# Optimization experiments

Measured on AMD Instinct MI355X. Metric: run time of the kernel, lower is better.

Reference implementation:

```python
import jax, jax.numpy as jnp
import numpy as np

B, S, D_IN, D_OUT = 4, 2048, 1024, 1024

def setup_inputs() -> dict:
    key = jax.random.key(0)
    k1, k2, k3, k4 = jax.random.split(key, 4)
    x = jax.random.normal(k1, (B, S, D_IN), dtype=jnp.float32)
    # torch Linear weight is [d_out, d_in]; store as [d_in, d_out] for x @ W
    scale = 1.0 / np.sqrt(D_IN)
    Wq = jax.random.normal(k2, (D_IN, D_OUT), dtype=jnp.float32) * scale
    Wk = jax.random.normal(k3, (D_IN, D_OUT), dtype=jnp.float32) * scale
    Wv = jax.random.normal(k4, (D_IN, D_OUT), dtype=jnp.float32) * scale
    return {"x": x, "Wq": Wq, "Wk": Wk, "Wv": Wv}

def reference(x, Wq, Wk, Wv):
    b, n, _ = x.shape
    q = jnp.einsum('bnd,de->bne', x, Wq)
    k = jnp.einsum('bnd,de->bne', x, Wk)
    v = jnp.einsum('bnd,de->bne', x, Wv)
    scores = jnp.einsum('bqe,bke->bqk', q, k) / jnp.sqrt(jnp.float32(k.shape[-1]))
    causal = jnp.tril(jnp.ones((n, n), dtype=bool))  # True = keep
    scores = jnp.where(causal[None], scores, -jnp.inf)
    attn = jax.nn.softmax(scores, axis=-1)
    # dropout p=0.0 -> identity (eval-equivalent)
    return jnp.einsum('bqk,bke->bqe', attn, v)
```

## Files before the change

kernel.cpp:

```cpp
#include <hip/hip_runtime.h>
#include <hip/hip_bf16.h>
#include <math.h>

typedef __hip_bfloat16 bf16;
typedef __attribute__((ext_vector_type(8))) short short8;
typedef __attribute__((ext_vector_type(4))) float f32x4;

#define GLD16(gp, lp)                                                          \
    __builtin_amdgcn_global_load_lds(                                          \
        (const __attribute__((address_space(1))) unsigned int*)(gp),           \
        (__attribute__((address_space(3))) unsigned int*)(lp), 16, 0, 0)


__global__ __launch_bounds__(256) void cvt_x(const float* __restrict__ in,
                                             bf16* __restrict__ out) {
    long base = ((long)blockIdx.x * 256 + threadIdx.x) * 8;
    const float4* p = (const float4*)(in + base);
    float4 a = p[0], b = p[1];
    union { bf16 h[8]; short8 v; } o;
    o.h[0] = __float2bfloat16(a.x); o.h[1] = __float2bfloat16(a.y);
    o.h[2] = __float2bfloat16(a.z); o.h[3] = __float2bfloat16(a.w);
    o.h[4] = __float2bfloat16(b.x); o.h[5] = __float2bfloat16(b.y);
    o.h[6] = __float2bfloat16(b.z); o.h[7] = __float2bfloat16(b.w);
    *(short8*)(out + base) = o.v;
}

__global__ __launch_bounds__(256) void cvt_w_t(const float* __restrict__ Wq,
                                               const float* __restrict__ Wk,
                                               const float* __restrict__ Wv,
                                               bf16* __restrict__ WT) {
    const float* W = blockIdx.z == 0 ? Wq : (blockIdx.z == 1 ? Wk : Wv);
    bf16* T = WT + (long)blockIdx.z * 1024 * 1024;
    __shared__ float t[32][33];
    int n0 = blockIdx.x * 32, k0 = blockIdx.y * 32;
    int tx = threadIdx.x, ty = threadIdx.y;
    #pragma unroll
    for (int i = 0; i < 4; ++i)
        t[ty * 4 + i][tx] = W[(long)(k0 + ty * 4 + i) * 1024 + n0 + tx];
    __syncthreads();
    #pragma unroll
    for (int i = 0; i < 4; ++i)
        T[(long)(n0 + ty * 4 + i) * 1024 + k0 + tx] =
            __float2bfloat16(t[tx][ty * 4 + i]);
}

template <int MODE>
__global__ __launch_bounds__(256) void gemm_bt(
    const bf16* __restrict__ A, const bf16* __restrict__ B,
    void* __restrict__ C0, void* __restrict__ C1, void* __restrict__ C2,
    float* __restrict__ RS, int lda, int ldb, float alpha, long az, long bz) {
    int tm, tn, bi = 0;
    if (MODE == 1) {
        tn = blockIdx.x; tm = blockIdx.y;
    } else if (MODE == 0) {
        int t = blockIdx.x % 136;
        bi = blockIdx.x / 136;
        int i = (int)((sqrtf(8.f * t + 1.f) - 1.f) * 0.5f);
        while ((i + 1) * (i + 2) / 2 <= t) ++i;
        while (i * (i + 1) / 2 > t) --i;
        tm = i; tn = t - i * (i + 1) / 2;
    } else {
        tm = 15 - (int)(blockIdx.x >> 5);
        int r = blockIdx.x & 31;
        tn = r & 7; bi = r >> 3;
    }
    const int nk = (MODE == 2) ? 2 * (tm + 1) : 16;
    A += (long)bi * az;
    B += (long)bi * bz;

    const int m0 = tm * 128, n0 = tn * 128;
    __shared__ bf16 As[128 * 64];
    __shared__ bf16 Bs[128 * 64];

    const int tid = threadIdx.x;
    const int wave = tid >> 6, lane = tid & 63;
    const int wr = wave >> 1, wc = wave & 1;
    const int lrow = lane & 15, kg = lane >> 4;

    f32x4 acc[4][4];
    #pragma unroll
    for (int i = 0; i < 4; ++i)
        #pragma unroll
        for (int j = 0; j < 4; ++j) acc[i][j] = (f32x4){0.f, 0.f, 0.f, 0.f};

    const int srow = tid >> 3;
    const int scol = (((tid & 7) ^ (srow & 7)) << 3);
    const bf16* ap = A + (long)(m0 + srow) * lda + scol;
    const bf16* bp = B + (long)(n0 + srow) * ldb + scol;
    char* asb = (char*)As + tid * 16;
    char* bsb = (char*)Bs + tid * 16;

    for (int t = 0; t < nk; ++t) {
        const int k0 = t << 6;
        GLD16(ap + k0, asb);
        GLD16(ap + 32L * lda + k0, asb + 4096);
        GLD16(ap + 64L * lda + k0, asb + 8192);
        GLD16(ap + 96L * lda + k0, asb + 12288);
        GLD16(bp + k0, bsb);
        GLD16(bp + 32L * ldb + k0, bsb + 4096);
        GLD16(bp + 64L * ldb + k0, bsb + 8192);
        GLD16(bp + 96L * ldb + k0, bsb + 12288);
        __syncthreads();
        #pragma unroll
        for (int kk = 0; kk < 2; ++kk) {
            short8 af[4], bfr[4];
            #pragma unroll
            for (int mi = 0; mi < 4; ++mi) {
                const int rr = wr * 64 + mi * 16 + lrow;
                const int ch = ((kk << 2) | kg) ^ (rr & 7);
                af[mi] = *(const short8*)(&As[rr * 64 + (ch << 3)]);
            }
            #pragma unroll
            for (int ni = 0; ni < 4; ++ni) {
                const int rr = wc * 64 + ni * 16 + lrow;
                const int ch = ((kk << 2) | kg) ^ (rr & 7);
                bfr[ni] = *(const short8*)(&Bs[rr * 64 + (ch << 3)]);
            }
            #pragma unroll
            for (int mi = 0; mi < 4; ++mi)
                #pragma unroll
                for (int ni = 0; ni < 4; ++ni)
                    acc[mi][ni] = __builtin_amdgcn_mfma_f32_16x16x32_bf16(
                        af[mi], bfr[ni], acc[mi][ni], 0, 0, 0);
        }
        __syncthreads();
    }

    const int rb = wr * 64 + (lane >> 4) * 4;
    const int cb = wc * 64 + (lane & 15);
    if (MODE == 0) {
        bf16* E = (bf16*)C0 + (long)bi * 4194304;
        float* rsb = RS + bi * 2048;
        #pragma unroll
        for (int mi = 0; mi < 4; ++mi)
            #pragma unroll
            for (int j = 0; j < 4; ++j) {
                const int gq = m0 + rb + mi * 16 + j;
                float rp = 0.f;
                #pragma unroll
                for (int ni = 0; ni < 4; ++ni) {
                    const int gk = n0 + cb + ni * 16;
                    float e = (gk <= gq) ? __expf(acc[mi][ni][j] * alpha) : 0.f;
                    E[(long)gq * 2048 + gk] = __float2bfloat16(e);
                    rp += e;
                }
                #pragma unroll
                for (int o = 1; o < 16; o <<= 1) rp += __shfl_xor(rp, o);
                if ((lane & 15) == 0) atomicAdd(rsb + gq, rp);
            }
    } else if (MODE == 2) {
        float* Cf = (float*)C0 + (long)bi * 2097152;
        const float* rsb = RS + bi * 2048;
        #pragma unroll
        for (int mi = 0; mi < 4; ++mi)
            #pragma unroll
            for (int j = 0; j < 4; ++j) {
                const int gq = m0 + rb + mi * 16 + j;
                const float inv = 1.f / rsb[gq];
                #pragma unroll
                for (int ni = 0; ni < 4; ++ni)
                    Cf[(long)gq * 1024 + (n0 + cb + ni * 16)] =
                        acc[mi][ni][j] * inv;
            }
    } else {
        const int sel = n0 >> 10;
        const int nb = n0 & 1023;
        if (sel < 2) {
            bf16* Cb = sel ? (bf16*)C1 : (bf16*)C0;
            #pragma unroll
            for (int mi = 0; mi < 4; ++mi)
                #pragma unroll
                for (int ni = 0; ni < 4; ++ni)
                    #pragma unroll
                    for (int j = 0; j < 4; ++j)
                        Cb[(long)(m0 + rb + mi * 16 + j) * 1024 + (nb + cb + ni * 16)] =
                            __float2bfloat16(acc[mi][ni][j]);
        } else {
            bf16* T = (bf16*)C2;
            #pragma unroll
            for (int mi = 0; mi < 4; ++mi)
                #pragma unroll
                for (int ni = 0; ni < 4; ++ni) {
                    int gm = m0 + rb + mi * 16;
                    int col = nb + cb + ni * 16;
                    int b = gm >> 11, mm = gm & 2047;
                    union { bf16 h[4]; ushort4 v; } o;
                    #pragma unroll
                    for (int j = 0; j < 4; ++j)
                        o.h[j] = __float2bfloat16(acc[mi][ni][j]);
                    *(ushort4*)(T + (long)b * 2097152 + (long)col * 2048 + mm) = o.v;
                }
        }
    }
}

extern "C" void kernel_launch(void* const* d_in, const int* in_sizes, int n_in,
                              void* d_out, int out_size, void* d_ws,
                              size_t ws_size, hipStream_t stream) {
    const float* x = (const float*)d_in[0];
    const float* Wq = (const float*)d_in[1];
    const float* Wk = (const float*)d_in[2];
    const float* Wv = (const float*)d_in[3];
    float* out = (float*)d_out;

    char* ws = (char*)d_ws;
    bf16* xb = (bf16*)ws;
    bf16* wt = (bf16*)(ws + 16777216);
    bf16* Qb = (bf16*)(ws + 23068672);
    bf16* Kb = (bf16*)(ws + 39845888);
    bf16* VT = (bf16*)(ws + 56623104);
    bf16* E  = (bf16*)(ws + 73400320);
    float* rs = (float*)(ws + 106954752);
    if (ws_size < 106987520) return;

    cvt_x<<<4096, 256, 0, stream>>>(x, xb);
    cvt_w_t<<<dim3(32, 32, 3), dim3(32, 8), 0, stream>>>(Wq, Wk, Wv, wt);
    hipMemsetAsync(rs, 0, 4 * 2048 * sizeof(float), stream);
    gemm_bt<1><<<dim3(24, 64), 256, 0, stream>>>(
        xb, wt, Qb, Kb, VT, nullptr, 1024, 1024, 1.f, 0, 0);
    gemm_bt<0><<<544, 256, 0, stream>>>(
        Qb, Kb, E, nullptr, nullptr, rs, 1024, 1024, 0.03125f, 2097152,
        2097152);
    gemm_bt<2><<<512, 256, 0, stream>>>(
        E, VT, out, nullptr, nullptr, rs, 2048, 2048, 1.f, 4194304, 2097152);
}
```

Before: 251.1 us.

## Use 512-thread 256x256 tiles with triple-buffered LDS pipeline in GEMMs

Measured after the change: 229.4 us. -8.6%, faster.

```diff
diff --git a/kernel.cpp b/kernel.cpp
--- a/kernel.cpp
+++ b/kernel.cpp
@@ -44,8 +44,8 @@
             __float2bfloat16(t[tx][ty * 4 + i]);
 }
 
-template <int MODE>
-__global__ __launch_bounds__(256) void gemm_bt(
+template <int MODE, int MF>
+__global__ __launch_bounds__(512, 2) void gemm8p(
     const bf16* __restrict__ A, const bf16* __restrict__ B,
     void* __restrict__ C0, void* __restrict__ C1, void* __restrict__ C2,
     float* __restrict__ RS, int lda, int ldb, float alpha, long az, long bz) {
@@ -53,86 +53,123 @@
     if (MODE == 1) {
         tn = blockIdx.x; tm = blockIdx.y;
     } else if (MODE == 0) {
-        int t = blockIdx.x % 136;
-        bi = blockIdx.x / 136;
+        int t = blockIdx.x % 36;
+        bi = blockIdx.x / 36;
         int i = (int)((sqrtf(8.f * t + 1.f) - 1.f) * 0.5f);
         while ((i + 1) * (i + 2) / 2 <= t) ++i;
         while (i * (i + 1) / 2 > t) --i;
         tm = i; tn = t - i * (i + 1) / 2;
     } else {
-        tm = 15 - (int)(blockIdx.x >> 5);
-        int r = blockIdx.x & 31;
-        tn = r & 7; bi = r >> 3;
+        tm = 15 - (int)(blockIdx.x >> 4);
+        int r = blockIdx.x & 15;
+        tn = r & 3; bi = r >> 2;
     }
-    const int nk = (MODE == 2) ? 2 * (tm + 1) : 16;
+    const int BM = MF * 32;
+    const int nk = (MODE == 2) ? 4 * (tm + 1) : 32;
     A += (long)bi * az;
     B += (long)bi * bz;
-
-    const int m0 = tm * 128, n0 = tn * 128;
-    __shared__ bf16 As[128 * 64];
-    __shared__ bf16 Bs[128 * 64];
+    const int m0 = tm * BM, n0 = tn * 256;
+
+    const int ABUF = MF * 1024;
+    __shared__ bf16 lds[3 * (MF * 1024 + 8192)];
+    bf16* Ab[3] = {lds, lds + ABUF, lds + 2 * ABUF};
+    bf16* Bb[3] = {lds + 3 * ABUF, lds + 3 * ABUF + 8192, lds + 3 * ABUF + 16384};
 
     const int tid = threadIdx.x;
     const int wave = tid >> 6, lane = tid & 63;
-    const int wr = wave >> 1, wc = wave & 1;
+    const int wr = wave >> 2, wc = wave & 3;
     const int lrow = lane & 15, kg = lane >> 4;
 
-    f32x4 acc[4][4];
+    f32x4 acc[MF][4];
     #pragma unroll
-    for (int i = 0; i < 4; ++i)
+    for (int i = 0; i < MF; ++i)
         #pragma unroll
         for (int j = 0; j < 4; ++j) acc[i][j] = (f32x4){0.f, 0.f, 0.f, 0.f};
 
-    const int srow = tid >> 3;
-    const int scol = (((tid & 7) ^ (srow & 7)) << 3);
+    const int srow = tid >> 2;
+    const int scol = ((((srow >> 1) & 3) ^ (tid & 3)) << 3);
     const bf16* ap = A + (long)(m0 + srow) * lda + scol;
     const bf16* bp = B + (long)(n0 + srow) * ldb + scol;
-    char* asb = (char*)As + tid * 16;
-    char* bsb = (char*)Bs + tid * 16;
+
+    #define STAGE_A(buf, kof)                                                  \
+        { char* d = (char*)(buf) + tid * 16;                                   \
+          GLD16(ap + (kof), d);                                                \
+          if (MF == 8) GLD16(ap + 128L * lda + (kof), d + 8192); }
+    #define STAGE_B(buf, kof)                                                  \
+        { char* d = (char*)(buf) + tid * 16;                                   \
+          GLD16(bp + (kof), d);                                                \
+          GLD16(bp + 128L * ldb + (kof), d + 8192); }
+
+    auto LDF = [&](const bf16* buf, int rr) {
+        return *(const short8*)(buf + rr * 32 + ((kg ^ ((rr >> 1) & 3)) << 3));
+    };
+
+    STAGE_A(Ab[0], 0); STAGE_B(Bb[0], 0);
+    STAGE_A(Ab[1], 32); STAGE_B(Bb[1], 32);
+
+    bf16 *acu = Ab[0], *anx = Ab[1], *ast = Ab[2];
+    bf16 *bcu = Bb[0], *bnx = Bb[1], *bst = Bb[2];
 
     for (int t = 0; t < nk; ++t) {
-        const int k0 = t << 6;
-        GLD16(ap + k0, asb);
-        GLD16(ap + 32L * lda + k0, asb + 4096);
-        GLD16(ap + 64L * lda + k0, asb + 8192);
-        GLD16(ap + 96L * lda + k0, asb + 12288);
-        GLD16(bp + k0, bsb);
-        GLD16(bp + 32L * ldb + k0, bsb + 4096);
-        GLD16(bp + 64L * ldb + k0, bsb + 8192);
-        GLD16(bp + 96L * ldb + k0, bsb + 12288);
-        __syncthreads();
-        #pragma unroll
-        for (int kk = 0; kk < 2; ++kk) {
-            short8 af[4], bfr[4];
-            #pragma unroll
-            for (int mi = 0; mi < 4; ++mi) {
-                const int rr = wr * 64 + mi * 16 + lrow;
-                const int ch = ((kk << 2) | kg) ^ (rr & 7);
-                af[mi] = *(const short8*)(&As[rr * 64 + (ch << 3)]);
-            }
-            #pragma unroll
-            for (int ni = 0; ni < 4; ++ni) {
-                const int rr = wc * 64 + ni * 16 + lrow;
-                const int ch = ((kk << 2) | kg) ^ (rr & 7);
-                bfr[ni] = *(const short8*)(&Bs[rr * 64 + (ch << 3)]);
-            }
+        if (t + 1 < nk) {
+            if (MF == 8) asm volatile("s_waitcnt vmcnt(4)" ::: "memory");
+            else         asm volatile("s_waitcnt vmcnt(3)" ::: "memory");
+        } else {
+            asm volatile("s_waitcnt vmcnt(0)" ::: "memory");
+        }
+        __builtin_amdgcn_s_barrier();
+        __builtin_amdgcn_sched_barrier(0);
+
+        const int kst = (t + 2) << 5;
+        const bool stg = (t + 2) < nk;
+        if (stg) { STAGE_A(ast, kst); if (MF == 4) STAGE_B(bst, kst); }
+
+        short8 bfr[4], af[4];
+        #pragma unroll
+        for (int ni = 0; ni < 4; ++ni)
+            bfr[ni] = LDF(bcu, wc * 64 + ni * 16 + lrow);
+        #pragma unroll
+        for (int mi = 0; mi < 4 && mi < MF; ++mi)
+            af[mi] = LDF(acu, wr * (MF * 16) + mi * 16 + lrow);
+        __builtin_amdgcn_s_setprio(1);
+        #pragma unroll
+        for (int mi = 0; mi < 4 && mi < MF; ++mi)
+            #pragma unroll
+            for (int ni = 0; ni < 4; ++ni)
+                acc[mi][ni] = __builtin_amdgcn_mfma_f32_16x16x32_bf16(
+                    af[mi], bfr[ni], acc[mi][ni], 0, 0, 0);
+        __builtin_amdgcn_s_setprio(0);
+
+        if (MF == 8) {
+            if (stg) STAGE_B(bst, kst);
+            short8 af2[4];
             #pragma unroll
             for (int mi = 0; mi < 4; ++mi)
+                af2[mi] = LDF(acu, wr * 128 + 64 + mi * 16 + lrow);
+            __builtin_amdgcn_s_setprio(1);
+            #pragma unroll
+            for (int mi = 0; mi < 4; ++mi)
                 #pragma unroll
                 for (int ni = 0; ni < 4; ++ni)
-                    acc[mi][ni] = __builtin_amdgcn_mfma_f32_16x16x32_bf16(
-                        af[mi], bfr[ni], acc[mi][ni], 0, 0, 0);
+                    acc[(MF == 8 ? mi + 4 : mi)][ni] =
+                        __builtin_amdgcn_mfma_f32_16x16x32_bf16(
+                            af2[mi], bfr[ni], acc[(MF == 8 ? mi + 4 : mi)][ni],
+                            0, 0, 0);
+            __builtin_amdgcn_s_setprio(0);
         }
-        __syncthreads();
+        bf16* ta = acu; acu = anx; anx = ast; ast = ta;
+        bf16* tb = bcu; bcu = bnx; bnx = bst; bst = tb;
     }
-
-    const int rb = wr * 64 + (lane >> 4) * 4;
+    #undef STAGE_A
+    #undef STAGE_B
+
+    const int rb = wr * (MF * 16) + (lane >> 4) * 4;
     const int cb = wc * 64 + (lane & 15);
     if (MODE == 0) {
         bf16* E = (bf16*)C0 + (long)bi * 4194304;
         float* rsb = RS + bi * 2048;
         #pragma unroll
-        for (int mi = 0; mi < 4; ++mi)
+        for (int mi = 0; mi < MF; ++mi)
             #pragma unroll
             for (int j = 0; j < 4; ++j) {
                 const int gq = m0 + rb + mi * 16 + j;
@@ -152,7 +189,7 @@
         float* Cf = (float*)C0 + (long)bi * 2097152;
         const float* rsb = RS + bi * 2048;
         #pragma unroll
-        for (int mi = 0; mi < 4; ++mi)
+        for (int mi = 0; mi < MF; ++mi)
             #pragma unroll
             for (int j = 0; j < 4; ++j) {
                 const int gq = m0 + rb + mi * 16 + j;
@@ -168,7 +205,7 @@
         if (sel < 2) {
             bf16* Cb = sel ? (bf16*)C1 : (bf16*)C0;
             #pragma unroll
-            for (int mi = 0; mi < 4; ++mi)
+            for (int mi = 0; mi < MF; ++mi)
                 #pragma unroll
                 for (int ni = 0; ni < 4; ++ni)
                     #pragma unroll
@@ -178,7 +215,7 @@
         } else {
             bf16* T = (bf16*)C2;
             #pragma unroll
-            for (int mi = 0; mi < 4; ++mi)
+            for (int mi = 0; mi < MF; ++mi)
                 #pragma unroll
                 for (int ni = 0; ni < 4; ++ni) {
                     int gm = m0 + rb + mi * 16;
@@ -216,11 +253,11 @@
     cvt_x<<<4096, 256, 0, stream>>>(x, xb);
     cvt_w_t<<<dim3(32, 32, 3), dim3(32, 8), 0, stream>>>(Wq, Wk, Wv, wt);
     hipMemsetAsync(rs, 0, 4 * 2048 * sizeof(float), stream);
-    gemm_bt<1><<<dim3(24, 64), 256, 0, stream>>>(
+    gemm8p<1, 8><<<dim3(12, 32), 512, 0, stream>>>(
         xb, wt, Qb, Kb, VT, nullptr, 1024, 1024, 1.f, 0, 0);
-    gemm_bt<0><<<544, 256, 0, stream>>>(
+    gemm8p<0, 8><<<144, 512, 0, stream>>>(
         Qb, Kb, E, nullptr, nullptr, rs, 1024, 1024, 0.03125f, 2097152,
         2097152);
-    gemm_bt<2><<<512, 256, 0, stream>>>(
+    gemm8p<2, 4><<<256, 512, 0, stream>>>(
         E, VT, out, nullptr, nullptr, rs, 2048, 2048, 1.f, 4194304, 2097152);
 }
```

## Triple-buffer GEMM staging with 512-thread blocks and paired causal tiles

Applied to the files above, without the earlier changes.

After: 225.8 us. -10.1%, faster.

```diff
diff --git a/kernel.cpp b/kernel.cpp
--- a/kernel.cpp
+++ b/kernel.cpp
@@ -44,153 +44,177 @@
             __float2bfloat16(t[tx][ty * 4 + i]);
 }
 
-template <int MODE>
-__global__ __launch_bounds__(256) void gemm_bt(
+template <int MODE, int MF>
+__global__ __launch_bounds__(512, 2) void gemmdp(
     const bf16* __restrict__ A, const bf16* __restrict__ B,
     void* __restrict__ C0, void* __restrict__ C1, void* __restrict__ C2,
     float* __restrict__ RS, int lda, int ldb, float alpha, long az, long bz) {
-    int tm, tn, bi = 0;
-    if (MODE == 1) {
-        tn = blockIdx.x; tm = blockIdx.y;
-    } else if (MODE == 0) {
-        int t = blockIdx.x % 136;
-        bi = blockIdx.x / 136;
-        int i = (int)((sqrtf(8.f * t + 1.f) - 1.f) * 0.5f);
-        while ((i + 1) * (i + 2) / 2 <= t) ++i;
-        while (i * (i + 1) / 2 > t) --i;
-        tm = i; tn = t - i * (i + 1) / 2;
-    } else {
-        tm = 15 - (int)(blockIdx.x >> 5);
-        int r = blockIdx.x & 31;
-        tn = r & 7; bi = r >> 3;
-    }
-    const int nk = (MODE == 2) ? 2 * (tm + 1) : 16;
-    A += (long)bi * az;
-    B += (long)bi * bz;
-
-    const int m0 = tm * 128, n0 = tn * 128;
-    __shared__ bf16 As[128 * 64];
-    __shared__ bf16 Bs[128 * 64];
+    constexpr int BM = MF * 64;
+    constexpr int S = MF * 4096 + 8192;
+    __shared__ bf16 lds[3 * S];
 
     const int tid = threadIdx.x;
     const int wave = tid >> 6, lane = tid & 63;
     const int wr = wave >> 1, wc = wave & 1;
     const int lrow = lane & 15, kg = lane >> 4;
-
-    f32x4 acc[4][4];
-    #pragma unroll
-    for (int i = 0; i < 4; ++i)
-        #pragma unroll
-        for (int j = 0; j < 4; ++j) acc[i][j] = (f32x4){0.f, 0.f, 0.f, 0.f};
-
+    const int s7 = lane & 7;
+
+    int tn, bi, tm0;
+    if (MODE == 1) {
+        tn = blockIdx.x; tm0 = blockIdx.y; bi = 0;
+    } else if (MODE == 0) {
+        int t = blockIdx.x % 72; bi = blockIdx.x / 72;
+        int m = (int)((sqrtf(4.f * t + 1.f) - 1.f) * 0.5f);
+        while ((m + 1) * (m + 2) <= t) ++m;
+        while (m * (m + 1) > t) --m;
+        tm0 = m; tn = t - m * (m + 1);
+    } else {
+        int r = blockIdx.x & 31;
+        tn = r & 7; bi = r >> 3; tm0 = blockIdx.x >> 5;
+    }
+    const bf16* Abase = A + (long)bi * az;
+    const bf16* Bbase = B + (long)bi * bz;
     const int srow = tid >> 3;
     const int scol = (((tid & 7) ^ (srow & 7)) << 3);
-    const bf16* ap = A + (long)(m0 + srow) * lda + scol;
-    const bf16* bp = B + (long)(n0 + srow) * ldb + scol;
-    char* asb = (char*)As + tid * 16;
-    char* bsb = (char*)Bs + tid * 16;
-
-    for (int t = 0; t < nk; ++t) {
-        const int k0 = t << 6;
-        GLD16(ap + k0, asb);
-        GLD16(ap + 32L * lda + k0, asb + 4096);
-        GLD16(ap + 64L * lda + k0, asb + 8192);
-        GLD16(ap + 96L * lda + k0, asb + 12288);
-        GLD16(bp + k0, bsb);
-        GLD16(bp + 32L * ldb + k0, bsb + 4096);
-        GLD16(bp + 64L * ldb + k0, bsb + 8192);
-        GLD16(bp + 96L * ldb + k0, bsb + 12288);
-        __syncthreads();
+    const int n0 = tn * 128;
+
+    const int NJOB = (MODE == 2) ? 2 : 1;
+    for (int job = 0; job < NJOB; ++job) {
+        const int tm = (MODE == 2 && job) ? 15 - tm0 : tm0;
+        const int m0 = tm * BM;
+        const int nk = (MODE == 2) ? 2 * (tm + 1) : 16;
+
+        const bf16* ap = Abase + (long)(m0 + srow) * lda + scol;
+        const bf16* bp = Bbase + (long)(n0 + srow) * ldb + scol;
+
+        f32x4 acc[MF][4];
         #pragma unroll
-        for (int kk = 0; kk < 2; ++kk) {
-            short8 af[4], bfr[4];
-            #pragma unroll
-            for (int mi = 0; mi < 4; ++mi) {
-                const int rr = wr * 64 + mi * 16 + lrow;
-                const int ch = ((kk << 2) | kg) ^ (rr & 7);
-                af[mi] = *(const short8*)(&As[rr * 64 + (ch << 3)]);
-            }
+        for (int i = 0; i < MF; ++i)
+            #pragma unroll
+            for (int j = 0; j < 4; ++j) acc[i][j] = (f32x4){0.f, 0.f, 0.f, 0.f};
+
+        #define STG(bb, k0)                                                    \
+            { char* d = (char*)(bb) + tid * 16;                                \
+              _Pragma("unroll")                                                \
+              for (int q = 0; q < MF; ++q)                                     \
+                  GLD16(ap + (long)(64 * q) * lda + (k0), d + q * 8192);       \
+              GLD16(bp + (k0), d + MF * 8192);                                 \
+              GLD16(bp + 64L * ldb + (k0), d + MF * 8192 + 8192); }
+
+        STG(lds, 0);
+        STG(lds + S, 64);
+        bf16 *cur = lds, *nxt = lds + S, *stg = lds + 2 * S;
+
+        for (int t = 0; t < nk; ++t) {
+            if (t + 1 < nk) {
+                if (MF == 4) asm volatile("s_waitcnt vmcnt(6)" ::: "memory");
+                else         asm volatile("s_waitcnt vmcnt(4)" ::: "memory");
+            } else {
+                asm volatile("s_waitcnt vmcnt(0)" ::: "memory");
+            }
+            __builtin_amdgcn_s_barrier();
+            __builtin_amdgcn_sched_barrier(0);
+            if (t + 2 < nk) STG(stg, (t + 2) << 6);
+
+            const bf16* ab = cur;
+            const bf16* bb = cur + MF * 4096;
+            short8 bq0[4], bq1[4];
             #pragma unroll
             for (int ni = 0; ni < 4; ++ni) {
                 const int rr = wc * 64 + ni * 16 + lrow;
-                const int ch = ((kk << 2) | kg) ^ (rr & 7);
-                bfr[ni] = *(const short8*)(&Bs[rr * 64 + (ch << 3)]);
-            }
-            #pragma unroll
-            for (int mi = 0; mi < 4; ++mi)
+                bq0[ni] = *(const short8*)(bb + rr * 64 + ((kg ^ s7) << 3));
+                bq1[ni] = *(const short8*)(bb + rr * 64 + (((4 | kg) ^ s7) << 3));
+            }
+            #pragma unroll
+            for (int mi = 0; mi < MF; ++mi) {
+                const int rr = wr * (MF * 16) + mi * 16 + lrow;
+                short8 a0 = *(const short8*)(ab + rr * 64 + ((kg ^ s7) << 3));
+                short8 a1 = *(const short8*)(ab + rr * 64 + (((4 | kg) ^ s7) << 3));
+                __builtin_amdgcn_s_setprio(1);
                 #pragma unroll
                 for (int ni = 0; ni < 4; ++ni)
                     acc[mi][ni] = __builtin_amdgcn_mfma_f32_16x16x32_bf16(
-                        af[mi], bfr[ni], acc[mi][ni], 0, 0, 0);
+                        a0, bq0[ni], acc[mi][ni], 0, 0, 0);
+                #pragma unroll
+                for (int ni = 0; ni < 4; ++ni)
+                    acc[mi][ni] = __builtin_amdgcn_mfma_f32_16x16x32_bf16(
+                        a1, bq1[ni], acc[mi][ni], 0, 0, 0);
+                __builtin_amdgcn_s_setprio(0);
+            }
+            bf16* tp = cur; cur = nxt; nxt = stg; stg = tp;
         }
-        __syncthreads();
-    }
-
-    const int rb = wr * 64 + (lane >> 4) * 4;
-    const int cb = wc * 64 + (lane & 15);
-    if (MODE == 0) {
-        bf16* E = (bf16*)C0 + (long)bi * 4194304;
-        float* rsb = RS + bi * 2048;
-        #pragma unroll
-        for (int mi = 0; mi < 4; ++mi)
-            #pragma unroll
-            for (int j = 0; j < 4; ++j) {
-                const int gq = m0 + rb + mi * 16 + j;
-                float rp = 0.f;
-                #pragma unroll
-                for (int ni = 0; ni < 4; ++ni) {
-                    const int gk = n0 + cb + ni * 16;
-                    float e = (gk <= gq) ? __expf(acc[mi][ni][j] * alpha) : 0.f;
-                    E[(long)gq * 2048 + gk] = __float2bfloat16(e);
-                    rp += e;
+        #undef STG
+
+        const int rb = wr * (MF * 16) + (lane >> 4) * 4;
+        const int cb = wc * 64 + lrow;
+        if (MODE == 0) {
+            bf16* E = (bf16*)C0 + (long)bi * 4194304;
+            float* rsb = RS + bi * 2048;
+            #pragma unroll
+            for (int mi = 0; mi < MF; ++mi)
+                #pragma unroll
+                for (int j = 0; j < 4; ++j) {
+                    const int gq = m0 + rb + mi * 16 + j;
+                    float rp = 0.f;
+                    #pragma unroll
+                    for (int ni = 0; ni < 4; ++ni) {
+                        const int gk = n0 + cb + ni * 16;
+                        float e = (gk <= gq) ? __expf(acc[mi][ni][j] * alpha) : 0.f;
+                        E[(long)gq * 2048 + gk] = __float2bfloat16(e);
+                        rp += e;
+                    }
+                    #pragma unroll
+                    for (int o = 1; o < 16; o <<= 1) rp += __shfl_xor(rp, o);
+                    if (lrow == 0) atomicAdd(rsb + gq, rp);
                 }
-                #pragma unroll
-                for (int o = 1; o < 16; o <<= 1) rp += __shfl_xor(rp, o);
-                if ((lane & 15) == 0) atomicAdd(rsb + gq, rp);
-            }
-    } else if (MODE == 2) {
-        float* Cf = (float*)C0 + (long)bi * 2097152;
-        const float* rsb = RS + bi * 2048;
-        #pragma unroll
-        for (int mi = 0; mi < 4; ++mi)
-            #pragma unroll
-            for (int j = 0; j < 4; ++j) {
-                const int gq = m0 + rb + mi * 16 + j;
-                const float inv = 1.f / rsb[gq];
-                #pragma unroll
-                for (int ni = 0; ni < 4; ++ni)
-                    Cf[(long)gq * 1024 + (n0 + cb + ni * 16)] =
-                        acc[mi][ni][j] * inv;
-            }
-    } else {
-        const int sel = n0 >> 10;
-        const int nb = n0 & 1023;
-        if (sel < 2) {
-            bf16* Cb = sel ? (bf16*)C1 : (bf16*)C0;
-            #pragma unroll
-            for (int mi = 0; mi < 4; ++mi)
-                #pragma unroll
-                for (int ni = 0; ni < 4; ++ni)
-                    #pragma unroll
-                    for (int j = 0; j < 4; ++j)
-                        Cb[(long)(m0 + rb + mi * 16 + j) * 1024 + (nb + cb + ni * 16)] =
-                            __float2bfloat16(acc[mi][ni][j]);
+        } else if (MODE == 2) {
+            float* Cf = (float*)C0 + (long)bi * 2097152;
+            const float* rsb = RS + bi * 2048;
+            #pragma unroll
+            for (int mi = 0; mi < MF; ++mi)
+                #pragma unroll
+                for (int j = 0; j < 4; ++j) {
+                    const int gq = m0 + rb + mi * 16 + j;
+                    const float inv = 1.f / rsb[gq];
+                    #pragma unroll
+                    for (int ni = 0; ni < 4; ++ni)
+                        Cf[(long)gq * 1024 + (n0 + cb + ni * 16)] =
+                            acc[mi][ni][j] * inv;
+                }
         } else {
-            bf16* T = (bf16*)C2;
-            #pragma unroll
-            for (int mi = 0; mi < 4; ++mi)
-                #pragma unroll
-                for (int ni = 0; ni < 4; ++ni) {
-                    int gm = m0 + rb + mi * 16;
-                    int col = nb + cb + ni * 16;
-                    int b = gm >> 11, mm = gm & 2047;
-                    union { bf16 h[4]; ushort4 v; } o;
-                    #pragma unroll
-                    for (int j = 0; j < 4; ++j)
-                        o.h[j] = __float2bfloat16(acc[mi][ni][j]);
-                    *(ushort4*)(T + (long)b * 2097152 + (long)col * 2048 + mm) = o.v;
-                }
+            const int sel = n0 >> 10;
+            const int nb = n0 & 1023;
+            if (sel < 2) {
+                bf16* Cb = sel ? (bf16*)C1 : (bf16*)C0;
+                #pragma unroll
+                for (int mi = 0; mi < MF; ++mi)
+                    #pragma unroll
+                    for (int ni = 0; ni < 4; ++ni)
+                        #pragma unroll
+                        for (int j = 0; j < 4; ++j)
+                            Cb[(long)(m0 + rb + mi * 16 + j) * 1024 +
+                               (nb + cb + ni * 16)] =
+                                __float2bfloat16(acc[mi][ni][j]);
+            } else {
+                bf16* T = (bf16*)C2;
+                #pragma unroll
+                for (int mi = 0; mi < MF; ++mi)
+                    #pragma unroll
+                    for (int ni = 0; ni < 4; ++ni) {
+                        int gm = m0 + rb + mi * 16;
+                        int col = nb + cb + ni * 16;
+                        int b = gm >> 11, mm = gm & 2047;
+                        union { bf16 h[4]; ushort4 v; } o;
+                        #pragma unroll
+                        for (int j = 0; j < 4; ++j)
+                            o.h[j] = __float2bfloat16(acc[mi][ni][j]);
+                        *(ushort4*)(T + (long)b * 2097152 + (long)col * 2048 + mm) =
+                            o.v;
+                    }
+            }
         }
+        if (MODE == 2 && job == 0)
+            __builtin_amdgcn_s_barrier();
     }
 }
 
@@ -216,11 +240,11 @@
     cvt_x<<<4096, 256, 0, stream>>>(x, xb);
     cvt_w_t<<<dim3(32, 32, 3), dim3(32, 8), 0, stream>>>(Wq, Wk, Wv, wt);
     hipMemsetAsync(rs, 0, 4 * 2048 * sizeof(float), stream);
-    gemm_bt<1><<<dim3(24, 64), 256, 0, stream>>>(
+    gemmdp<1, 4><<<dim3(24, 32), 512, 0, stream>>>(
         xb, wt, Qb, Kb, VT, nullptr, 1024, 1024, 1.f, 0, 0);
-    gemm_bt<0><<<544, 256, 0, stream>>>(
+    gemmdp<0, 4><<<288, 512, 0, stream>>>(
         Qb, Kb, E, nullptr, nullptr, rs, 1024, 1024, 0.03125f, 2097152,
         2097152);
-    gemm_bt<2><<<512, 256, 0, stream>>>(
+    gemmdp<2, 2><<<256, 512, 0, stream>>>(
         E, VT, out, nullptr, nullptr, rs, 2048, 2048, 1.f, 4194304, 2097152);
 }
```
